# Performance work log

Hardware: AMD Instinct MI355X
Metric: run time of the kernel (lower is better)

Reference implementation:

```python
import jax, jax.numpy as jnp
import numpy as np

N, C, H, W = 4, 256, 64, 64  # in_channels == out_channels == C


def conv1x1(x, w, b):
    # x: [N, Cin, H, W], w: [Cout, Cin], b: [Cout]
    return jnp.einsum('nchw,oc->nohw', x, w) + b[None, :, None, None]


def setup_inputs() -> dict:
    key = jax.random.key(0)
    ks = jax.random.split(key, 4)
    scale = 1.0 / np.sqrt(C)
    return {
        'x': jax.random.normal(ks[0], (N, C, H, W), dtype=jnp.float32),
        'theta_w': jax.random.normal(ks[1], (C, C), dtype=jnp.float32) * scale,
        'theta_b': jnp.zeros((C,), dtype=jnp.float32),
        'phi_w': jax.random.normal(ks[2], (C, C), dtype=jnp.float32) * scale,
        'phi_b': jnp.zeros((C,), dtype=jnp.float32),
        'conv1_w': jax.random.normal(ks[3], (C, C), dtype=jnp.float32) * scale,
        'conv1_b': jnp.zeros((C,), dtype=jnp.float32),
    }


def reference(x, theta_w, theta_b, phi_w, phi_b, conv1_w, conv1_b):
    n, c, h, w = x.shape
    hw = h * w
    theta = conv1x1(x, theta_w, theta_b).reshape(n, c, hw)   # queries [N,C,HW]
    phi = conv1x1(x, phi_w, phi_b).reshape(n, c, hw)         # keys    [N,C,HW]
    g = x.reshape(n, c, hw)                                   # values  [N,C,HW]
    # f = einsum('niab,nicd->nabcd') flattened: [N, HW_q, HW_k]
    scores = jnp.einsum('ncp,ncq->npq', theta, phi) / jnp.sqrt(jnp.asarray(c, x.dtype))
    attn = jax.nn.softmax(scores, axis=-1)                    # softmax over keys
    # f = einsum('nabcd,nicd->niab'): weighted sum of values
    f = jnp.einsum('npq,ncq->ncp', attn, g).reshape(n, c, h, w)
    result = conv1x1(f, conv1_w, conv1_b)
    return x + result
```

## Files before the change

### kernel.cpp

```cpp
#include <hip/hip_runtime.h>
#include <hip/hip_bf16.h>

typedef __attribute__((ext_vector_type(8))) short short8;
typedef __attribute__((ext_vector_type(4))) short short4_t;
typedef __attribute__((ext_vector_type(4))) float float4_t;
typedef unsigned short ushort;

#define HW 4096
#define CC 256
#define NBATCH 4
#define SEQ ((size_t)NBATCH * HW)

static __device__ __forceinline__ unsigned short f2b(float f) {
    union { float f; unsigned u; } v; v.f = f;
    unsigned r = v.u + 0x7FFF + ((v.u >> 16) & 1);
    return (unsigned short)(r >> 16);
}
static __device__ __forceinline__ float b2f(unsigned short u) {
    union { unsigned u; float f; } v; v.u = ((unsigned)u) << 16;
    return v.f;
}
static __device__ __forceinline__ unsigned pk2(float a, float b) {
    __hip_bfloat162 h = __float22bfloat162_rn(make_float2(a, b));
    union { __hip_bfloat162 h; unsigned u; } v; v.h = h; return v.u;
}

__global__ __launch_bounds__(512)
void k_pp(const float* __restrict__ x,
          const float* __restrict__ tw, const float* __restrict__ pw,
          const float* __restrict__ thb, const float* __restrict__ phb,
          unsigned short* __restrict__ gb,
          unsigned short* __restrict__ thT, unsigned short* __restrict__ phT) {
    __shared__ float T[64][65];
    __shared__ __align__(16) ushort F[64][256];
    const int n = blockIdx.z;
    const int p0 = blockIdx.x * 64;
    const int tid = threadIdx.x;

    {
        const int pl = tid & 63, rg = tid >> 6;
        for (int cc = 0; cc < 4; cc++) {
            const int c0 = cc * 64;
            const float* xp = x + ((size_t)n * CC + c0) * HW + p0;
            #pragma unroll
            for (int i = 0; i < 8; i++) {
                int cl = rg * 8 + i;
                float v = xp[(size_t)cl * HW + pl];
                T[cl][pl] = v;
                gb[((size_t)n * CC + c0 + cl) * HW + p0 + pl] = f2b(v);
            }
            __syncthreads();
            const int cl2 = tid & 63, pg = tid >> 6;
            #pragma unroll
            for (int i = 0; i < 8; i++) {
                int plw = pg * 8 + i;
                int c = c0 + cl2;
                int swz = (c >> 3) ^ (plw & 7);
                F[plw][swz * 8 + (c & 7)] = f2b(T[cl2][plw]);
            }
            __syncthreads();
        }
    }

    const int w = tid >> 6, lane = tid & 63;
    const int nidx = lane & 15, quad = lane >> 4;
    const float* Wsel = (w < 4) ? tw : pw;
    const float* bsel = (w < 4) ? thb : phb;
    unsigned short* osel = (w < 4) ? thT : phT;
    const int cq = w & 3;

    float4_t acc[4][4];
    #pragma unroll
    for (int i = 0; i < 4; i++)
        #pragma unroll
        for (int j = 0; j < 4; j++) acc[i][j] = (float4_t)(0.f);

    for (int ks = 0; ks < 8; ks++) {
        short8 af[4];
        #pragma unroll
        for (int mt = 0; mt < 4; mt++) {
            int row = mt * 16 + nidx;
            int chn = (ks * 4 + quad) ^ (row & 7);
            af[mt] = *(const short8*)(&F[row][chn * 8]);
        }
        #pragma unroll
        for (int cb = 0; cb < 4; cb++) {
            int co = cq * 64 + cb * 16 + nidx;
            const float* wp = Wsel + (size_t)co * CC + ks * 32 + quad * 8;
            float4_t w0 = *(const float4_t*)(wp);
            float4_t w1 = *(const float4_t*)(wp + 4);
            union { short8 s; unsigned u[4]; } bfr;
            bfr.u[0] = pk2(w0[0], w0[1]); bfr.u[1] = pk2(w0[2], w0[3]);
            bfr.u[2] = pk2(w1[0], w1[1]); bfr.u[3] = pk2(w1[2], w1[3]);
            #pragma unroll
            for (int mt = 0; mt < 4; mt++)
                acc[mt][cb] = __builtin_amdgcn_mfma_f32_16x16x32_bf16(af[mt], bfr.s, acc[mt][cb], 0, 0, 0);
        }
    }

    #pragma unroll
    for (int cb = 0; cb < 4; cb++) {
        int co = cq * 64 + cb * 16 + nidx;
        float bias = bsel[co];
        #pragma unroll
        for (int mt = 0; mt < 4; mt++)
            #pragma unroll
            for (int r = 0; r < 4; r++) {
                size_t prow = (size_t)n * HW + p0 + mt * 16 + quad * 4 + r;
                osel[prow * CC + co] = f2b(acc[mt][cb][r] + bias);
            }
    }
}

__global__ __launch_bounds__(512)
void k_attn(const unsigned short* __restrict__ thetaT,
            const unsigned short* __restrict__ phiT,
            const unsigned short* __restrict__ gb,
            ushort* __restrict__ Ow, float* __restrict__ lw) {
    __shared__ __align__(16) ushort Kl[2][16384];
    __shared__ __align__(16) ushort Pbuf[2][16][64][8];
    __shared__ float Lbuf[2][128];

    const int tid = threadIdx.x;
    const int w = tid >> 6, lane = tid & 63;
    const int nidx = lane & 15, quad = lane >> 4;
    const int qg = w & 3;
    const int kh = w >> 2;
    const int nb = (blockIdx.x & 7) >> 1;
    const int h  = blockIdx.x & 1;
    const int qtile = blockIdx.x >> 3;
    const int p0 = qtile * 128;
    const size_t seq0 = (size_t)nb * HW;
    const ushort* Kg = phiT + seq0 * CC;
    const ushort* Vg = gb + (size_t)nb * CC * HW;
    const int k00 = h * 2048;

    short8 th[2][8];
    #pragma unroll
    for (int qs = 0; qs < 2; qs++) {
        const ushort* qrow = thetaT + (seq0 + p0 + qg * 32 + qs * 16 + nidx) * CC + quad * 8;
        #pragma unroll
        for (int kb = 0; kb < 8; kb++) th[qs][kb] = *(const short8*)(qrow + kb * 32);
    }

    float4_t o[2][8];
    #pragma unroll
    for (int i = 0; i < 2; i++)
        #pragma unroll
        for (int j = 0; j < 8; j++) o[i][j] = (float4_t)(0.f);
    float lrow[2] = {0.f, 0.f};

    const int c_s = tid >> 4, n_s = tid & 15;
    const int kfbase = (c_s >> 2) * 512 + ((c_s & 3) * 16 + n_s) * 8;
    auto loadKregs = [&](short8 (&kr)[4], int tt) {
        #pragma unroll
        for (int rr = 0; rr < 4; rr++)
            kr[rr] = *(const short8*)(Kg + (size_t)(k00 + tt * 64 + rr * 16 + n_s) * CC + c_s * 8);
    };
    auto stageK = [&](int buf, const short8 (&kr)[4]) {
        #pragma unroll
        for (int rr = 0; rr < 4; rr++) *(short8*)(&Kl[buf][rr * 4096 + kfbase]) = kr[rr];
    };
    auto loadVregs = [&](short8 (&vr)[4], int tt) {
        #pragma unroll
        for (int mg = 0; mg < 2; mg++)
            #pragma unroll
            for (int kst = 0; kst < 2; kst++)
                vr[mg * 2 + kst] = *(const short8*)(Vg + (size_t)(w * 32 + mg * 16 + nidx) * HW
                                                    + k00 + tt * 64 + kst * 32 + quad * 8);
    };

    const float SC = 0.0625f * 1.44269504088896f;
    const int Gp = quad >> 1;
    const int pcell_lo = (nidx ^ (Gp * 4));
    const int pj0 = (quad & 1) * 4;
    const int prcell = ((lane >> 4) << 4) | ((lane & 15) ^ (((lane >> 4) & 1) * 4));

    float4_t s00, s01, s10, s11;
    auto expPhase = [&](int buf) {
        {
            float e0 = exp2f(s00[0] * SC), e1 = exp2f(s00[1] * SC);
            float e2 = exp2f(s00[2] * SC), e3 = exp2f(s00[3] * SC);
            lrow[0] += (e0 + e1) + (e2 + e3);
            uint2 pk; pk.x = pk2(e0, e1); pk.y = pk2(e2, e3);
            *(uint2*)(&Pbuf[buf][(qg * 2 + 0) * 2 + kh][(0 * 2 + Gp) * 16 + pcell_lo][pj0]) = pk;
        }
        {
            float e0 = exp2f(s01[0] * SC), e1 = exp2f(s01[1] * SC);
            float e2 = exp2f(s01[2] * SC), e3 = exp2f(s01[3] * SC);
            lrow[1] += (e0 + e1) + (e2 + e3);
            uint2 pk; pk.x = pk2(e0, e1); pk.y = pk2(e2, e3);
            *(uint2*)(&Pbuf[buf][(qg * 2 + 1) * 2 + kh][(0 * 2 + Gp) * 16 + pcell_lo][pj0]) = pk;
        }
        {
            float e0 = exp2f(s10[0] * SC), e1 = exp2f(s10[1] * SC);
            float e2 = exp2f(s10[2] * SC), e3 = exp2f(s10[3] * SC);
            lrow[0] += (e0 + e1) + (e2 + e3);
            uint2 pk; pk.x = pk2(e0, e1); pk.y = pk2(e2, e3);
            *(uint2*)(&Pbuf[buf][(qg * 2 + 0) * 2 + kh][(1 * 2 + Gp) * 16 + pcell_lo][pj0]) = pk;
        }
        {
            float e0 = exp2f(s11[0] * SC), e1 = exp2f(s11[1] * SC);
            float e2 = exp2f(s11[2] * SC), e3 = exp2f(s11[3] * SC);
            lrow[1] += (e0 + e1) + (e2 + e3);
            uint2 pk; pk.x = pk2(e0, e1); pk.y = pk2(e2, e3);
            *(uint2*)(&Pbuf[buf][(qg * 2 + 1) * 2 + kh][(1 * 2 + Gp) * 16 + pcell_lo][pj0]) = pk;
        }
    };

    short8 kregs[4], vA[4], vB[4];

    auto ITER = [&](int t, const short8 (&vCur)[4], short8 (&vNext)[4]) {
        const int pb = t & 1;
        const int kbuf = (t + 1) & 1;
        s00 = (float4_t)(0.f); s01 = (float4_t)(0.f);
        s10 = (float4_t)(0.f); s11 = (float4_t)(0.f);
        #pragma unroll
        for (int i = 0; i < 8; i++) {
            short8 k0 = *(const short8*)(&Kl[kbuf][((kh * 2 + 0) * 8 + i) * 512 + lane * 8]);
            short8 k1 = *(const short8*)(&Kl[kbuf][((kh * 2 + 1) * 8 + i) * 512 + lane * 8]);
            s00 = __builtin_amdgcn_mfma_f32_16x16x32_bf16(k0, th[0][i], s00, 0, 0, 0);
            s01 = __builtin_amdgcn_mfma_f32_16x16x32_bf16(k0, th[1][i], s01, 0, 0, 0);
            s10 = __builtin_amdgcn_mfma_f32_16x16x32_bf16(k1, th[0][i], s10, 0, 0, 0);
            s11 = __builtin_amdgcn_mfma_f32_16x16x32_bf16(k1, th[1][i], s11, 0, 0, 0);
            short8 pf0 = *(const short8*)(&Pbuf[pb][i * 2 + 0][prcell][0]);
            short8 pf1 = *(const short8*)(&Pbuf[pb][i * 2 + 1][prcell][0]);
            o[0][i] = __builtin_amdgcn_mfma_f32_16x16x32_bf16(vCur[0], pf0, o[0][i], 0, 0, 0);
            o[0][i] = __builtin_amdgcn_mfma_f32_16x16x32_bf16(vCur[1], pf1, o[0][i], 0, 0, 0);
            o[1][i] = __builtin_amdgcn_mfma_f32_16x16x32_bf16(vCur[2], pf0, o[1][i], 0, 0, 0);
            o[1][i] = __builtin_amdgcn_mfma_f32_16x16x32_bf16(vCur[3], pf1, o[1][i], 0, 0, 0);
        }
        loadVregs(vNext, t + 1);
        expPhase((t + 1) & 1);
        if (t < 30) {
            stageK((t + 2) & 1, kregs);
            loadKregs(kregs, (t + 3 < 32) ? t + 3 : 31);
        }
        __syncthreads();
    };

    loadKregs(kregs, 0); loadVregs(vA, 0);
    stageK(0, kregs);
    loadKregs(kregs, 1);
    __syncthreads();
    s00 = (float4_t)(0.f); s01 = (float4_t)(0.f); s10 = (float4_t)(0.f); s11 = (float4_t)(0.f);
    #pragma unroll
    for (int kb = 0; kb < 8; kb++) {
        short8 k0 = *(const short8*)(&Kl[0][((kh * 2 + 0) * 8 + kb) * 512 + lane * 8]);
        short8 k1 = *(const short8*)(&Kl[0][((kh * 2 + 1) * 8 + kb) * 512 + lane * 8]);
        s00 = __builtin_amdgcn_mfma_f32_16x16x32_bf16(k0, th[0][kb], s00, 0, 0, 0);
        s01 = __builtin_amdgcn_mfma_f32_16x16x32_bf16(k0, th[1][kb], s01, 0, 0, 0);
        s10 = __builtin_amdgcn_mfma_f32_16x16x32_bf16(k1, th[0][kb], s10, 0, 0, 0);
        s11 = __builtin_amdgcn_mfma_f32_16x16x32_bf16(k1, th[1][kb], s11, 0, 0, 0);
    }
    expPhase(0);
    stageK(1, kregs);
    loadKregs(kregs, 2);
    __syncthreads();

    #pragma unroll 1
    for (int tt = 0; tt < 15; tt++) {
        ITER(tt * 2, vA, vB);
        ITER(tt * 2 + 1, vB, vA);
    }
    ITER(30, vA, vB);
    #pragma unroll
    for (int i = 0; i < 8; i++) {
        short8 pf0 = *(const short8*)(&Pbuf[1][i * 2 + 0][prcell][0]);
        short8 pf1 = *(const short8*)(&Pbuf[1][i * 2 + 1][prcell][0]);
        o[0][i] = __builtin_amdgcn_mfma_f32_16x16x32_bf16(vB[0], pf0, o[0][i], 0, 0, 0);
        o[0][i] = __builtin_amdgcn_mfma_f32_16x16x32_bf16(vB[1], pf1, o[0][i], 0, 0, 0);
        o[1][i] = __builtin_amdgcn_mfma_f32_16x16x32_bf16(vB[2], pf0, o[1][i], 0, 0, 0);
        o[1][i] = __builtin_amdgcn_mfma_f32_16x16x32_bf16(vB[3], pf1, o[1][i], 0, 0, 0);
    }

    #pragma unroll
    for (int qs = 0; qs < 2; qs++) {
        float v = lrow[qs];
        v += __shfl_xor(v, 16);
        v += __shfl_xor(v, 32);
        if (quad == 0) Lbuf[kh][qg * 32 + qs * 16 + nidx] = v;
    }
    __syncthreads();
    if (tid < 128)
        lw[(size_t)h * SEQ + seq0 + p0 + tid] = Lbuf[0][tid] + Lbuf[1][tid];
    ushort* Op = Ow + ((size_t)h * SEQ + seq0 + p0) * CC;
    #pragma unroll
    for (int mg = 0; mg < 2; mg++)
        #pragma unroll
        for (int qq = 0; qq < 8; qq++) {
            uint2 pk;
            pk.x = pk2(o[mg][qq][0], o[mg][qq][1]);
            pk.y = pk2(o[mg][qq][2], o[mg][qq][3]);
            *(uint2*)(Op + (size_t)(qq * 16 + nidx) * CC + w * 32 + mg * 16 + quad * 4) = pk;
        }
}

__global__ __launch_bounds__(512)
void k_final(const float* __restrict__ cw,
             const float* __restrict__ bc,
             const ushort* __restrict__ Ow,
             const float* __restrict__ lw,
             const float* __restrict__ x,
             float* __restrict__ out) {
    __shared__ __align__(16) ushort F[64][256];
    const int n = blockIdx.z;
    const int p0 = blockIdx.x * 64;
    const int tid = threadIdx.x;

    {
        const int r = tid >> 3;
        const int c0 = tid & 7;
        const size_t grow = (size_t)n * HW + p0 + r;
        const float li = 1.0f / (lw[grow] + lw[SEQ + grow]);
        const short8* O0 = (const short8*)(Ow + grow * CC);
        const short8* O1 = (const short8*)(Ow + SEQ * CC + grow * CC);
        #pragma unroll
        for (int i = 0; i < 4; i++) {
            int ch = c0 + 8 * i;
            short8 a = O0[ch];
            short8 b = O1[ch];
            union { short8 s; unsigned u[4]; } pk;
            float f[8];
            #pragma unroll
            for (int j = 0; j < 8; j++)
                f[j] = (b2f((ushort)a[j]) + b2f((ushort)b[j])) * li;
            pk.u[0] = pk2(f[0], f[1]); pk.u[1] = pk2(f[2], f[3]);
            pk.u[2] = pk2(f[4], f[5]); pk.u[3] = pk2(f[6], f[7]);
            int swz = ch ^ (r & 7);
            *(short8*)(&F[r][swz * 8]) = pk.s;
        }
    }
    __syncthreads();

    const int w = tid >> 6, lane = tid & 63;
    const int nidx = lane & 15, quad = lane >> 4;
    const int co_base = w * 32;
    float4_t acc[2][4];
    #pragma unroll
    for (int i = 0; i < 2; i++)
        #pragma unroll
        for (int j = 0; j < 4; j++) acc[i][j] = (float4_t)(0.f);

    const float* a0row = cw + (size_t)(co_base + nidx) * CC + quad * 8;
    const float* a1row = cw + (size_t)(co_base + 16 + nidx) * CC + quad * 8;
    for (int ks = 0; ks < 8; ks++) {
        float4_t w00 = *(const float4_t*)(a0row + ks * 32);
        float4_t w01 = *(const float4_t*)(a0row + ks * 32 + 4);
        float4_t w10 = *(const float4_t*)(a1row + ks * 32);
        float4_t w11 = *(const float4_t*)(a1row + ks * 32 + 4);
        union { short8 s; unsigned u[4]; } a0, a1;
        a0.u[0] = pk2(w00[0], w00[1]); a0.u[1] = pk2(w00[2], w00[3]);
        a0.u[2] = pk2(w01[0], w01[1]); a0.u[3] = pk2(w01[2], w01[3]);
        a1.u[0] = pk2(w10[0], w10[1]); a1.u[1] = pk2(w10[2], w10[3]);
        a1.u[2] = pk2(w11[0], w11[1]); a1.u[3] = pk2(w11[2], w11[3]);
        #pragma unroll
        for (int pb = 0; pb < 4; pb++) {
            int row = pb * 16 + nidx;
            int chunk = (ks * 4 + quad) ^ (row & 7);
            short8 bb = *(const short8*)(&F[row][chunk * 8]);
            acc[0][pb] = __builtin_amdgcn_mfma_f32_16x16x32_bf16(a0.s, bb, acc[0][pb], 0, 0, 0);
            acc[1][pb] = __builtin_amdgcn_mfma_f32_16x16x32_bf16(a1.s, bb, acc[1][pb], 0, 0, 0);
        }
    }

    #pragma unroll
    for (int cb = 0; cb < 2; cb++) {
        #pragma unroll
        for (int pb = 0; pb < 4; pb++) {
            #pragma unroll
            for (int r2 = 0; r2 < 4; r2++) {
                int co = co_base + cb * 16 + quad * 4 + r2;
                size_t idx = ((size_t)n * CC + co) * HW + p0 + pb * 16 + nidx;
                out[idx] = x[idx] + bc[co] + acc[cb][pb][r2];
            }
        }
    }
}

extern "C" void kernel_launch(void* const* d_in, const int* in_sizes, int n_in,
                              void* d_out, int out_size, void* d_ws, size_t ws_size,
                              hipStream_t stream) {
    const float* x       = (const float*)d_in[0];
    const float* theta_w = (const float*)d_in[1];
    const float* theta_b = (const float*)d_in[2];
    const float* phi_w   = (const float*)d_in[3];
    const float* phi_b   = (const float*)d_in[4];
    const float* conv1_w = (const float*)d_in[5];
    const float* conv1_b = (const float*)d_in[6];
    float* out = (float*)d_out;

    unsigned short* gb  = (unsigned short*)d_ws;
    unsigned short* thT = gb  + SEQ * CC;
    unsigned short* phT = thT + SEQ * CC;
    unsigned short* Ow  = phT + SEQ * CC;
    float* lw = (float*)(Ow + 2 * SEQ * CC);

    k_pp<<<dim3(64, 1, 4), 512, 0, stream>>>(x, theta_w, phi_w, theta_b, phi_b, gb, thT, phT);
    k_attn<<<dim3(256), 512, 0, stream>>>(thT, phT, gb, Ow, lw);
    k_final<<<dim3(64, 1, 4), 512, 0, stream>>>(conv1_w, conv1_b, Ow, lw, x, out);
}
```

Before: 185.1 us.

## Halve attention query and key tiles to double grid size and occupancy

```diff
diff --git a/kernel.cpp b/kernel.cpp
--- a/kernel.cpp
+++ b/kernel.cpp
@@ -2,7 +2,6 @@
 #include <hip/hip_bf16.h>
 
 typedef __attribute__((ext_vector_type(8))) short short8;
-typedef __attribute__((ext_vector_type(4))) short short4_t;
 typedef __attribute__((ext_vector_type(4))) float float4_t;
 typedef unsigned short ushort;
 
@@ -112,14 +111,14 @@
     }
 }
 
-__global__ __launch_bounds__(512)
+__global__ __launch_bounds__(512, 4)
 void k_attn(const unsigned short* __restrict__ thetaT,
             const unsigned short* __restrict__ phiT,
             const unsigned short* __restrict__ gb,
             ushort* __restrict__ Ow, float* __restrict__ lw) {
-    __shared__ __align__(16) ushort Kl[2][16384];
-    __shared__ __align__(16) ushort Pbuf[2][16][64][8];
-    __shared__ float Lbuf[2][128];
+    __shared__ __align__(16) ushort Kl[2][8192];
+    __shared__ __align__(16) ushort Pbuf[2][4][64][8];
+    __shared__ float Lbuf[2][64];
 
     const int tid = threadIdx.x;
     const int w = tid >> 6, lane = tid & 63;
@@ -129,45 +128,42 @@
     const int nb = (blockIdx.x & 7) >> 1;
     const int h  = blockIdx.x & 1;
     const int qtile = blockIdx.x >> 3;
-    const int p0 = qtile * 128;
+    const int p0 = qtile * 64;
     const size_t seq0 = (size_t)nb * HW;
     const ushort* Kg = phiT + seq0 * CC;
     const ushort* Vg = gb + (size_t)nb * CC * HW;
     const int k00 = h * 2048;
 
-    short8 th[2][8];
-    #pragma unroll
-    for (int qs = 0; qs < 2; qs++) {
-        const ushort* qrow = thetaT + (seq0 + p0 + qg * 32 + qs * 16 + nidx) * CC + quad * 8;
-        #pragma unroll
-        for (int kb = 0; kb < 8; kb++) th[qs][kb] = *(const short8*)(qrow + kb * 32);
-    }
-
-    float4_t o[2][8];
+    short8 th[8];
+    {
+        const ushort* qrow = thetaT + (seq0 + p0 + qg * 16 + nidx) * CC + quad * 8;
+        #pragma unroll
+        for (int kb = 0; kb < 8; kb++) th[kb] = *(const short8*)(qrow + kb * 32);
+    }
+
+    float4_t o[2][4];
     #pragma unroll
     for (int i = 0; i < 2; i++)
         #pragma unroll
-        for (int j = 0; j < 8; j++) o[i][j] = (float4_t)(0.f);
-    float lrow[2] = {0.f, 0.f};
+        for (int j = 0; j < 4; j++) o[i][j] = (float4_t)(0.f);
+    float lrow = 0.f;
 
     const int c_s = tid >> 4, n_s = tid & 15;
     const int kfbase = (c_s >> 2) * 512 + ((c_s & 3) * 16 + n_s) * 8;
-    auto loadKregs = [&](short8 (&kr)[4], int tt) {
-        #pragma unroll
-        for (int rr = 0; rr < 4; rr++)
-            kr[rr] = *(const short8*)(Kg + (size_t)(k00 + tt * 64 + rr * 16 + n_s) * CC + c_s * 8);
-    };
-    auto stageK = [&](int buf, const short8 (&kr)[4]) {
-        #pragma unroll
-        for (int rr = 0; rr < 4; rr++) *(short8*)(&Kl[buf][rr * 4096 + kfbase]) = kr[rr];
-    };
-    auto loadVregs = [&](short8 (&vr)[4], int tt) {
+    auto loadKregs = [&](short8 (&kr)[2], int tt) {
+        #pragma unroll
+        for (int rr = 0; rr < 2; rr++)
+            kr[rr] = *(const short8*)(Kg + (size_t)(k00 + tt * 32 + rr * 16 + n_s) * CC + c_s * 8);
+    };
+    auto stageK = [&](int buf, const short8 (&kr)[2]) {
+        #pragma unroll
+        for (int rr = 0; rr < 2; rr++) *(short8*)(&Kl[buf][rr * 4096 + kfbase]) = kr[rr];
+    };
+    auto loadVregs = [&](short8 (&vr)[2], int tt) {
         #pragma unroll
         for (int mg = 0; mg < 2; mg++)
-            #pragma unroll
-            for (int kst = 0; kst < 2; kst++)
-                vr[mg * 2 + kst] = *(const short8*)(Vg + (size_t)(w * 32 + mg * 16 + nidx) * HW
-                                                    + k00 + tt * 64 + kst * 32 + quad * 8);
+            vr[mg] = *(const short8*)(Vg + (size_t)(w * 32 + mg * 16 + nidx) * HW
+                                      + k00 + tt * 32 + quad * 8);
     };
 
     const float SC = 0.0625f * 1.44269504088896f;
@@ -176,65 +172,36 @@
     const int pj0 = (quad & 1) * 4;
     const int prcell = ((lane >> 4) << 4) | ((lane & 15) ^ (((lane >> 4) & 1) * 4));
 
-    float4_t s00, s01, s10, s11;
+    float4_t s0;
     auto expPhase = [&](int buf) {
-        {
-            float e0 = exp2f(s00[0] * SC), e1 = exp2f(s00[1] * SC);
-            float e2 = exp2f(s00[2] * SC), e3 = exp2f(s00[3] * SC);
-            lrow[0] += (e0 + e1) + (e2 + e3);
-            uint2 pk; pk.x = pk2(e0, e1); pk.y = pk2(e2, e3);
-            *(uint2*)(&Pbuf[buf][(qg * 2 + 0) * 2 + kh][(0 * 2 + Gp) * 16 + pcell_lo][pj0]) = pk;
-        }
-        {
-            float e0 = exp2f(s01[0] * SC), e1 = exp2f(s01[1] * SC);
-            float e2 = exp2f(s01[2] * SC), e3 = exp2f(s01[3] * SC);
-            lrow[1] += (e0 + e1) + (e2 + e3);
-            uint2 pk; pk.x = pk2(e0, e1); pk.y = pk2(e2, e3);
-            *(uint2*)(&Pbuf[buf][(qg * 2 + 1) * 2 + kh][(0 * 2 + Gp) * 16 + pcell_lo][pj0]) = pk;
-        }
-        {
-            float e0 = exp2f(s10[0] * SC), e1 = exp2f(s10[1] * SC);
-            float e2 = exp2f(s10[2] * SC), e3 = exp2f(s10[3] * SC);
-            lrow[0] += (e0 + e1) + (e2 + e3);
-            uint2 pk; pk.x = pk2(e0, e1); pk.y = pk2(e2, e3);
-            *(uint2*)(&Pbuf[buf][(qg * 2 + 0) * 2 + kh][(1 * 2 + Gp) * 16 + pcell_lo][pj0]) = pk;
-        }
-        {
-            float e0 = exp2f(s11[0] * SC), e1 = exp2f(s11[1] * SC);
-            float e2 = exp2f(s11[2] * SC), e3 = exp2f(s11[3] * SC);
-            lrow[1] += (e0 + e1) + (e2 + e3);
-            uint2 pk; pk.x = pk2(e0, e1); pk.y = pk2(e2, e3);
-            *(uint2*)(&Pbuf[buf][(qg * 2 + 1) * 2 + kh][(1 * 2 + Gp) * 16 + pcell_lo][pj0]) = pk;
-        }
-    };
-
-    short8 kregs[4], vA[4], vB[4];
-
-    auto ITER = [&](int t, const short8 (&vCur)[4], short8 (&vNext)[4]) {
+        float e0 = exp2f(s0[0] * SC), e1 = exp2f(s0[1] * SC);
+        float e2 = exp2f(s0[2] * SC), e3 = exp2f(s0[3] * SC);
+        lrow += (e0 + e1) + (e2 + e3);
+        uint2 pk; pk.x = pk2(e0, e1); pk.y = pk2(e2, e3);
+        *(uint2*)(&Pbuf[buf][qg][(kh * 2 + Gp) * 16 + pcell_lo][pj0]) = pk;
+    };
+
+    short8 kregs[2], vA[2], vB[2];
+
+    auto ITER = [&](int t, const short8 (&vCur)[2], short8 (&vNext)[2]) {
         const int pb = t & 1;
         const int kbuf = (t + 1) & 1;
-        s00 = (float4_t)(0.f); s01 = (float4_t)(0.f);
-        s10 = (float4_t)(0.f); s11 = (float4_t)(0.f);
+        s0 = (float4_t)(0.f);
         #pragma unroll
         for (int i = 0; i < 8; i++) {
-            short8 k0 = *(const short8*)(&Kl[kbuf][((kh * 2 + 0) * 8 + i) * 512 + lane * 8]);
-            short8 k1 = *(const short8*)(&Kl[kbuf][((kh * 2 + 1) * 8 + i) * 512 + lane * 8]);
-            s00 = __builtin_amdgcn_mfma_f32_16x16x32_bf16(k0, th[0][i], s00, 0, 0, 0);
-            s01 = __builtin_amdgcn_mfma_f32_16x16x32_bf16(k0, th[1][i], s01, 0, 0, 0);
-            s10 = __builtin_amdgcn_mfma_f32_16x16x32_bf16(k1, th[0][i], s10, 0, 0, 0);
-            s11 = __builtin_amdgcn_mfma_f32_16x16x32_bf16(k1, th[1][i], s11, 0, 0, 0);
-            short8 pf0 = *(const short8*)(&Pbuf[pb][i * 2 + 0][prcell][0]);
-            short8 pf1 = *(const short8*)(&Pbuf[pb][i * 2 + 1][prcell][0]);
-            o[0][i] = __builtin_amdgcn_mfma_f32_16x16x32_bf16(vCur[0], pf0, o[0][i], 0, 0, 0);
-            o[0][i] = __builtin_amdgcn_mfma_f32_16x16x32_bf16(vCur[1], pf1, o[0][i], 0, 0, 0);
-            o[1][i] = __builtin_amdgcn_mfma_f32_16x16x32_bf16(vCur[2], pf0, o[1][i], 0, 0, 0);
-            o[1][i] = __builtin_amdgcn_mfma_f32_16x16x32_bf16(vCur[3], pf1, o[1][i], 0, 0, 0);
+            short8 k0 = *(const short8*)(&Kl[kbuf][(kh * 8 + i) * 512 + lane * 8]);
+            s0 = __builtin_amdgcn_mfma_f32_16x16x32_bf16(k0, th[i], s0, 0, 0, 0);
+            if (i < 4) {
+                short8 pf = *(const short8*)(&Pbuf[pb][i][prcell][0]);
+                o[0][i] = __builtin_amdgcn_mfma_f32_16x16x32_bf16(vCur[0], pf, o[0][i], 0, 0, 0);
+                o[1][i] = __builtin_amdgcn_mfma_f32_16x16x32_bf16(vCur[1], pf, o[1][i], 0, 0, 0);
+            }
         }
         loadVregs(vNext, t + 1);
         expPhase((t + 1) & 1);
-        if (t < 30) {
+        if (t < 62) {
             stageK((t + 2) & 1, kregs);
-            loadKregs(kregs, (t + 3 < 32) ? t + 3 : 31);
+            loadKregs(kregs, (t + 3 < 64) ? t + 3 : 63);
         }
         __syncthreads();
     };
@@ -243,15 +210,11 @@
     stageK(0, kregs);
     loadKregs(kregs, 1);
     __syncthreads();
-    s00 = (float4_t)(0.f); s01 = (float4_t)(0.f); s10 = (float4_t)(0.f); s11 = (float4_t)(0.f);
+    s0 = (float4_t)(0.f);
     #pragma unroll
     for (int kb = 0; kb < 8; kb++) {
-        short8 k0 = *(const short8*)(&Kl[0][((kh * 2 + 0) * 8 + kb) * 512 + lane * 8]);
-        short8 k1 = *(const short8*)(&Kl[0][((kh * 2 + 1) * 8 + kb) * 512 + lane * 8]);
-        s00 = __builtin_amdgcn_mfma_f32_16x16x32_bf16(k0, th[0][kb], s00, 0, 0, 0);
-        s01 = __builtin_amdgcn_mfma_f32_16x16x32_bf16(k0, th[1][kb], s01, 0, 0, 0);
-        s10 = __builtin_amdgcn_mfma_f32_16x16x32_bf16(k1, th[0][kb], s10, 0, 0, 0);
-        s11 = __builtin_amdgcn_mfma_f32_16x16x32_bf16(k1, th[1][kb], s11, 0, 0, 0);
+        short8 k0 = *(const short8*)(&Kl[0][(kh * 8 + kb) * 512 + lane * 8]);
+        s0 = __builtin_amdgcn_mfma_f32_16x16x32_bf16(k0, th[kb], s0, 0, 0, 0);
     }
     expPhase(0);
     stageK(1, kregs);
@@ -259,40 +222,36 @@
     __syncthreads();
 
     #pragma unroll 1
-    for (int tt = 0; tt < 15; tt++) {
+    for (int tt = 0; tt < 31; tt++) {
         ITER(tt * 2, vA, vB);
         ITER(tt * 2 + 1, vB, vA);
     }
-    ITER(30, vA, vB);
-    #pragma unroll
-    for (int i = 0; i < 8; i++) {
-        short8 pf0 = *(const short8*)(&Pbuf[1][i * 2 + 0][prcell][0]);
-        short8 pf1 = *(const short8*)(&Pbuf[1][i * 2 + 1][prcell][0]);
-        o[0][i] = __builtin_amdgcn_mfma_f32_16x16x32_bf16(vB[0], pf0, o[0][i], 0, 0, 0);
-        o[0][i] = __builtin_amdgcn_mfma_f32_16x16x32_bf16(vB[1], pf1, o[0][i], 0, 0, 0);
-        o[1][i] = __builtin_amdgcn_mfma_f32_16x16x32_bf16(vB[2], pf0, o[1][i], 0, 0, 0);
-        o[1][i] = __builtin_amdgcn_mfma_f32_16x16x32_bf16(vB[3], pf1, o[1][i], 0, 0, 0);
-    }
-
-    #pragma unroll
-    for (int qs = 0; qs < 2; qs++) {
-        float v = lrow[qs];
+    ITER(62, vA, vB);
+    #pragma unroll
+    for (int i = 0; i < 4; i++) {
+        short8 pf = *(const short8*)(&Pbuf[1][i][prcell][0]);
+        o[0][i] = __builtin_amdgcn_mfma_f32_16x16x32_bf16(vB[0], pf, o[0][i], 0, 0, 0);
+        o[1][i] = __builtin_amdgcn_mfma_f32_16x16x32_bf16(vB[1], pf, o[1][i], 0, 0, 0);
+    }
+
+    {
+        float v = lrow;
         v += __shfl_xor(v, 16);
         v += __shfl_xor(v, 32);
-        if (quad == 0) Lbuf[kh][qg * 32 + qs * 16 + nidx] = v;
+        if (quad == 0) Lbuf[kh][qg * 16 + nidx] = v;
     }
     __syncthreads();
-    if (tid < 128)
+    if (tid < 64)
         lw[(size_t)h * SEQ + seq0 + p0 + tid] = Lbuf[0][tid] + Lbuf[1][tid];
     ushort* Op = Ow + ((size_t)h * SEQ + seq0 + p0) * CC;
     #pragma unroll
     for (int mg = 0; mg < 2; mg++)
         #pragma unroll
-        for (int qq = 0; qq < 8; qq++) {
+        for (int i = 0; i < 4; i++) {
             uint2 pk;
-            pk.x = pk2(o[mg][qq][0], o[mg][qq][1]);
-            pk.y = pk2(o[mg][qq][2], o[mg][qq][3]);
-            *(uint2*)(Op + (size_t)(qq * 16 + nidx) * CC + w * 32 + mg * 16 + quad * 4) = pk;
+            pk.x = pk2(o[mg][i][0], o[mg][i][1]);
+            pk.y = pk2(o[mg][i][2], o[mg][i][3]);
+            *(uint2*)(Op + (size_t)(i * 16 + nidx) * CC + w * 32 + mg * 16 + quad * 4) = pk;
         }
 }
 
@@ -397,6 +356,6 @@
     float* lw = (float*)(Ow + 2 * SEQ * CC);
 
     k_pp<<<dim3(64, 1, 4), 512, 0, stream>>>(x, theta_w, phi_w, theta_b, phi_b, gb, thT, phT);
-    k_attn<<<dim3(256), 512, 0, stream>>>(thT, phT, gb, Ow, lw);
+    k_attn<<<dim3(512), 512, 0, stream>>>(thT, phT, gb, Ow, lw);
     k_final<<<dim3(64, 1, 4), 512, 0, stream>>>(conv1_w, conv1_b, Ow, lw, x, out);
 }
```

Result: slower. 235.1 us (+27.0%).
